# Kernel tuning notes

Hardware: AMD Instinct MI355X
Metric: run time of the kernel (lower is better)

## Reference

```python
import jax, jax.numpy as jnp
import numpy as np

N, E, B = 50000, 800000, 2000
EMB, FEAT, L, NTASK = 300, 512, 5, 1
EPS = 1e-5


def setup_inputs() -> dict:
    key = jax.random.key(0)
    ks = jax.random.split(key, 40)
    s = 0.05
    d = {
        'x': jax.random.randint(ks[0], (N, 42), 0, 3),
        'edge_index': jax.random.randint(ks[1], (2, E), 0, N),
        'edge_attr': jax.random.randint(ks[2], (E, 10), 0, 3),
        'batch': jnp.sort(jax.random.randint(ks[3], (N,), 0, B)),
        'x_add': jax.random.normal(ks[4], (B, 200), jnp.float32),
        # atom embeddings
        'atom_e1': jax.random.normal(ks[5], (120, EMB), jnp.float32) * s,
        'atom_e2': jax.random.normal(ks[6], (3, EMB), jnp.float32) * s,
        'atom_w3': jax.random.normal(ks[7], (40, EMB), jnp.float32) * s,
        'atom_b3': jnp.zeros((EMB,), jnp.float32),
        # per-layer GINEConv params (stacked over L layers)
        'edge_e1': jax.random.normal(ks[8], (L, 6, EMB), jnp.float32) * s,
        'edge_e2': jax.random.normal(ks[9], (L, 4, EMB), jnp.float32) * s,
        'edge_w3': jax.random.normal(ks[10], (L, 8, EMB), jnp.float32) * s,
        'edge_b3': jnp.zeros((L, EMB), jnp.float32),
        'mlp_w1': jax.random.normal(ks[11], (L, EMB, 2 * EMB), jnp.float32) * s,
        'mlp_b1': jnp.zeros((L, 2 * EMB), jnp.float32),
        'mlp_w2': jax.random.normal(ks[12], (L, 2 * EMB, EMB), jnp.float32) * s,
        'mlp_b2': jnp.zeros((L, EMB), jnp.float32),
        'bn_g': jnp.ones((L, EMB), jnp.float32),
        'bn_b': jnp.zeros((L, EMB), jnp.float32),
        # feat_lin: emb_dim + 200 -> feat_dim
        'feat_w': jax.random.normal(ks[13], (EMB + 200, FEAT), jnp.float32) * s,
        'feat_b': jnp.zeros((FEAT,), jnp.float32),
        # pred head: 512->256 softplus, 256->256 softplus, 256->1
        'pw1': jax.random.normal(ks[14], (FEAT, FEAT // 2), jnp.float32) * s,
        'pb1': jnp.zeros((FEAT // 2,), jnp.float32),
        'pw2': jax.random.normal(ks[15], (FEAT // 2, FEAT // 2), jnp.float32) * s,
        'pb2': jnp.zeros((FEAT // 2,), jnp.float32),
        'pw3': jax.random.normal(ks[16], (FEAT // 2, NTASK), jnp.float32) * s,
        'pb3': jnp.zeros((NTASK,), jnp.float32),
    }
    return d


def reference(x, edge_index, edge_attr, batch, x_add,
              atom_e1, atom_e2, atom_w3, atom_b3,
              edge_e1, edge_e2, edge_w3, edge_b3,
              mlp_w1, mlp_b1, mlp_w2, mlp_b2, bn_g, bn_b,
              feat_w, feat_b, pw1, pb1, pw2, pb2, pw3, pb3):
    n = x.shape[0]
    nb = x_add.shape[0]

    # node embedding: emb(atom_type) + emb(chirality) + Linear(40 float feats)
    h = (atom_e1[x[:, 0]] + atom_e2[x[:, 1]]
         + x[:, 2:].astype(jnp.float32) @ atom_w3 + atom_b3)

    # add self loops once (same for every layer); self-loop attr: col0=4, rest 0
    loop = jnp.arange(n, dtype=edge_index.dtype)
    src = jnp.concatenate([edge_index[0], loop])
    dst = jnp.concatenate([edge_index[1], loop])
    ea0 = jnp.concatenate([edge_attr[:, 0], jnp.full((n,), 4, edge_attr.dtype)])
    ea1 = jnp.concatenate([edge_attr[:, 1], jnp.zeros((n,), edge_attr.dtype)])
    eaf = jnp.concatenate([edge_attr[:, 2:].astype(jnp.float32),
                           jnp.zeros((n, 8), jnp.float32)], axis=0)

    for l in range(L):
        e_emb = edge_e1[l][ea0] + edge_e2[l][ea1] + eaf @ edge_w3[l] + edge_b3[l]
        msg = h[src] + e_emb                              # [E+N, EMB] gather
        agg = jax.ops.segment_sum(msg, dst, num_segments=n)  # scatter-add
        h = jnp.maximum(agg @ mlp_w1[l] + mlp_b1[l], 0.0) @ mlp_w2[l] + mlp_b2[l]
        # BatchNorm1d (training-mode batch stats, biased var)
        mu = jnp.mean(h, axis=0)
        var = jnp.mean((h - mu) ** 2, axis=0)
        h = (h - mu) * jax.lax.rsqrt(var + EPS) * bn_g[l] + bn_b[l]
        if l != L - 1:
            h = jnp.maximum(h, 0.0)
    h_node = h

    # global mean pool per graph
    sums = jax.ops.segment_sum(h_node, batch, num_segments=nb)
    cnt = jax.ops.segment_sum(jnp.ones((n, 1), h_node.dtype), batch, num_segments=nb)
    pooled = sums / jnp.maximum(cnt, 1.0)

    g = jnp.concatenate([pooled, x_add], axis=1) @ feat_w + feat_b
    g = jax.nn.softplus(g @ pw1 + pb1)
    g = jax.nn.softplus(g @ pw2 + pb2)
    pred = g @ pw3 + pb3
    return h_node, pred
```

## Files before the change

kernel.cpp:

```cpp
#include <hip/hip_runtime.h>
#include <stdint.h>

#define NN 50000
#define EE 800000
#define BG 2000
#define EMB 300
#define HP 320
#define YP 640
#define MPAD 50048
#define MHEAD 2048
#define NLAYER 5

typedef __attribute__((ext_vector_type(8))) _Float16 f16x8;
typedef __attribute__((ext_vector_type(4))) float f32x4;

__device__ __forceinline__ _Float16 f2h(float f) { return (_Float16)f; }

__global__ void k_tconv_all(const float* __restrict__ mw1, const float* __restrict__ mw2,
        const float* __restrict__ fw, const float* __restrict__ pw1, const float* __restrict__ pw2,
        _Float16* __restrict__ w1t, _Float16* __restrict__ w2t, _Float16* __restrict__ fwt,
        _Float16* __restrict__ p1t, _Float16* __restrict__ p2t) {
    int job = blockIdx.x;
    const float* src; _Float16* dst; int K, Ns, Kp, Np;
    if (job < 5)       { src = mw1 + (size_t)job * EMB * 2 * EMB; dst = w1t + (size_t)job * YP * HP; K = EMB; Ns = 2 * EMB; Kp = HP; Np = YP; }
    else if (job < 10) { int l = job - 5; src = mw2 + (size_t)l * 2 * EMB * EMB; dst = w2t + (size_t)l * HP * YP; K = 2 * EMB; Ns = EMB; Kp = YP; Np = HP; }
    else if (job == 10){ src = fw;  dst = fwt; K = 500; Ns = 512; Kp = 512; Np = 512; }
    else if (job == 11){ src = pw1; dst = p1t; K = 512; Ns = 256; Kp = 512; Np = 256; }
    else               { src = pw2; dst = p2t; K = 256; Ns = 256; Kp = 256; Np = 256; }
    int total = Kp * Np;
    for (int idx = blockIdx.y * 256 + threadIdx.x; idx < total; idx += gridDim.y * 256) {
        int n = idx / Kp, k = idx - n * Kp;
        float v = (n < Ns && k < K) ? src[(size_t)k * Ns + n] : 0.f;
        dst[idx] = f2h(v);
    }
}

__global__ void k_padbias_all(const float* __restrict__ mb1, const float* __restrict__ mb2,
                              float* __restrict__ b1p, float* __restrict__ b2p) {
    int idx = blockIdx.x * 256 + threadIdx.x;
    if (idx < NLAYER * YP) {
        int l = idx / YP, c = idx - l * YP;
        b1p[idx] = (c < 2 * EMB) ? mb1[(size_t)l * 2 * EMB + c] : 0.f;
    } else if (idx < NLAYER * YP + NLAYER * HP) {
        int j = idx - NLAYER * YP; int l = j / HP, c = j - l * HP;
        b2p[j] = (c < EMB) ? mb2[(size_t)l * EMB + c] : 0.f;
    }
}

__global__ void k_prep(int* __restrict__ deg, int* __restrict__ cursor,
                       float* __restrict__ psum, float* __restrict__ psq,
                       float* __restrict__ scl, float* __restrict__ sft) {
    int i = blockIdx.x * blockDim.x + threadIdx.x;
    if (i < NN) { deg[i] = 0; cursor[i] = 0; }
    if (i < HP) { psum[i] = 0.f; psq[i] = 0.f; scl[i] = 1.f; sft[i] = 0.f; }
}

__global__ __launch_bounds__(320) void k_embed(const int* __restrict__ x,
        const float* __restrict__ ae1, const float* __restrict__ ae2,
        const float* __restrict__ aw3, const float* __restrict__ ab3,
        _Float16* __restrict__ h2) {
    int i = blockIdx.x, tid = threadIdx.x;
    __shared__ int sx[42];
    if (tid < 42) sx[tid] = x[(size_t)i * 42 + tid];
    __syncthreads();
    if (tid < EMB) {
        float v = ab3[tid] + ae1[(size_t)sx[0] * EMB + tid] + ae2[(size_t)sx[1] * EMB + tid];
        #pragma unroll 8
        for (int j = 0; j < 40; j++) v += (float)sx[2 + j] * aw3[(size_t)j * EMB + tid];
        h2[(size_t)i * HP + tid] = f2h(v);
    } else {
        h2[(size_t)i * HP + tid] = (_Float16)0.f;
    }
}

__global__ void k_deg(const int* __restrict__ ei, int* __restrict__ deg) {
    int e = blockIdx.x * blockDim.x + threadIdx.x;
    if (e < EE) atomicAdd(&deg[ei[EE + e]], 1);
}

__global__ __launch_bounds__(1024) void k_scan(const int* __restrict__ deg,
                                               int* __restrict__ rowptr) {
    __shared__ int part[1024];
    int t = threadIdx.x;
    const int chunk = (NN + 1023) / 1024;
    int i0 = t * chunk;
    int i1 = min(i0 + chunk, NN);
    int s = 0;
    for (int i = i0; i < i1; i++) s += deg[i];
    part[t] = s;
    __syncthreads();
    for (int off = 1; off < 1024; off <<= 1) {
        int v = part[t];
        int u = (t >= off) ? part[t - off] : 0;
        __syncthreads();
        part[t] = v + u;
        __syncthreads();
    }
    int run = (t > 0) ? part[t - 1] : 0;
    for (int i = i0; i < i1; i++) { rowptr[i] = run; run += deg[i]; }
    if (t == 1023) rowptr[NN] = part[1023];
}

__global__ void k_fill(const int* __restrict__ ei, const int* __restrict__ ea,
                       const int* __restrict__ rowptr, int* __restrict__ cursor,
                       int* __restrict__ col, unsigned int* __restrict__ eattr) {
    int e = blockIdx.x * blockDim.x + threadIdx.x;
    if (e < EE) {
        int d = ei[EE + e];
        int pos = rowptr[d] + atomicAdd(&cursor[d], 1);
        col[pos] = ei[e];
        unsigned int p = (unsigned int)ea[e * 10 + 0] | ((unsigned int)ea[e * 10 + 1] << 2);
        #pragma unroll
        for (int j = 0; j < 8; j++) p |= (unsigned int)ea[e * 10 + 2 + j] << (4 + 2 * j);
        eattr[pos] = p;
    }
}

__global__ __launch_bounds__(256) void k_stats(const int* __restrict__ rowptr,
        const unsigned int* __restrict__ eattr, int* __restrict__ stat) {
    int node = blockIdx.x * 4 + (threadIdx.x >> 6);
    int lane = threadIdx.x & 63;
    if (node >= NN) return;
    int beg = rowptr[node], end = rowptr[node + 1];
    int c0 = 0, c1 = 0, c2 = 0, d1 = 0, d2 = 0;
    int s[8] = {0, 0, 0, 0, 0, 0, 0, 0};
    for (int e = beg + lane; e < end; e += 64) {
        unsigned int p = eattr[e];
        unsigned int a0 = p & 3u, a1 = (p >> 2) & 3u;
        c0 += (a0 == 0); c1 += (a0 == 1); c2 += (a0 == 2);
        d1 += (a1 == 1); d2 += (a1 == 2);
        #pragma unroll
        for (int j = 0; j < 8; j++) s[j] += (int)((p >> (4 + 2 * j)) & 3u);
    }
    #pragma unroll
    for (int off = 32; off; off >>= 1) {
        c0 += __shfl_down(c0, off); c1 += __shfl_down(c1, off); c2 += __shfl_down(c2, off);
        d1 += __shfl_down(d1, off); d2 += __shfl_down(d2, off);
        #pragma unroll
        for (int j = 0; j < 8; j++) s[j] += __shfl_down(s[j], off);
    }
    if (lane == 0) {
        int dg = end - beg;
        int* st = stat + (size_t)node * 20;
        st[0] = c0; st[1] = c1; st[2] = c2; st[3] = 0; st[4] = 1; st[5] = 0;
        st[6] = dg - d1 - d2 + 1; st[7] = d1; st[8] = d2; st[9] = 0;
        #pragma unroll
        for (int j = 0; j < 8; j++) st[10 + j] = s[j];
        st[18] = dg + 1; st[19] = 0;
    }
}

__global__ __launch_bounds__(320) void k_agg(const _Float16* __restrict__ h2,
        const float* __restrict__ scl, const float* __restrict__ sft, int dorelu,
        const int* __restrict__ stat, const int* __restrict__ rowptr,
        const int* __restrict__ col,
        const float* __restrict__ ee1, const float* __restrict__ ee2,
        const float* __restrict__ ew3, const float* __restrict__ eb3,
        _Float16* __restrict__ agg, int layer) {
    int i = blockIdx.x;
    int tid = threadIdx.x;
    if (i >= NN) { agg[(size_t)i * HP + tid] = (_Float16)0.f; return; }
    __shared__ int ss[20];
    if (tid < 20) ss[tid] = stat[(size_t)i * 20 + tid];
    float sc_ = scl[tid], sf_ = sft[tid];
    __syncthreads();
    int c = tid;
    bool act = c < EMB;
    float acc = 0.f;
    if (act) {
        const float* e1 = ee1 + (size_t)layer * 6 * EMB;
        const float* e2 = ee2 + (size_t)layer * 4 * EMB;
        const float* w3 = ew3 + (size_t)layer * 8 * EMB;
        float v = eb3[(size_t)layer * EMB + c] * (float)ss[18];
        #pragma unroll
        for (int k = 0; k < 6; k++) v += (float)ss[k] * e1[k * EMB + c];
        #pragma unroll
        for (int k = 0; k < 4; k++) v += (float)ss[6 + k] * e2[k * EMB + c];
        #pragma unroll
        for (int j = 0; j < 8; j++) v += (float)ss[10 + j] * w3[j * EMB + c];
        float hv = (float)h2[(size_t)i * HP + c];
        float t = fmaf(hv, sc_, sf_);
        if (dorelu) t = fmaxf(t, 0.f);
        acc = v + t;
        int beg = rowptr[i], end = rowptr[i + 1];
        #pragma unroll 4
        for (int e = beg; e < end; ++e) {
            int sid = col[e];
            float v2 = (float)h2[(size_t)sid * HP + c];
            float t2 = fmaf(v2, sc_, sf_);
            if (dorelu) t2 = fmaxf(t2, 0.f);
            acc += t2;
        }
    }
    agg[(size_t)i * HP + tid] = act ? f2h(acc) : (_Float16)0.f;
}

__global__ __launch_bounds__(256) void k_gemm(const _Float16* __restrict__ A, int lda,
        const _Float16* __restrict__ Wt, int ldw, const float* __restrict__ bias,
        _Float16* __restrict__ C, int ldc, int K, int act,
        float* __restrict__ psum, float* __restrict__ psq) {
    __shared__ _Float16 As[128 * 32];
    __shared__ _Float16 Bs[64 * 32];
    int tid = threadIdx.x;
    int lane = tid & 63;
    int wid = tid >> 6;
    int wr = wid >> 1, wc = wid & 1;
    size_t rowBase = (size_t)blockIdx.x * 128;
    int colBase = blockIdx.y * 64;

    int srow = tid >> 2;
    int schunk = tid & 3;
    const _Float16* Ab  = A + (rowBase + srow) * (size_t)lda + (schunk << 3);
    const _Float16* Ab2 = Ab + (size_t)64 * lda;
    const _Float16* Bb  = Wt + ((size_t)colBase + srow) * ldw + (schunk << 3);
    int swz = ((schunk ^ ((srow >> 1) & 3)) << 3);
    int wa0 = srow * 32 + swz;
    int wa1 = wa0 + 64 * 32;
    int wb  = wa0;

    uint4 ra0 = *(const uint4*)Ab;
    uint4 ra1 = *(const uint4*)Ab2;
    uint4 rb  = *(const uint4*)Bb;

    int lr = lane & 15, lg = lane >> 4;
    int lswz = (lr >> 1) & 3;
    int aoff[4], boff[2];
    #pragma unroll
    for (int m = 0; m < 4; m++) { int r = wr * 64 + m * 16 + lr; aoff[m] = r * 32 + ((lg ^ lswz) << 3); }
    #pragma unroll
    for (int n = 0; n < 2; n++) { int r = wc * 32 + n * 16 + lr; boff[n] = r * 32 + ((lg ^ lswz) << 3); }

    f32x4 acc[4][2];
    #pragma unroll
    for (int m = 0; m < 4; m++)
        #pragma unroll
        for (int n = 0; n < 2; n++) acc[m][n] = (f32x4){0.f, 0.f, 0.f, 0.f};

    int nk = K >> 5;
    for (int kt = 0; kt < nk; ++kt) {
        __syncthreads();
        *(uint4*)&As[wa0] = ra0;
        *(uint4*)&As[wa1] = ra1;
        *(uint4*)&Bs[wb]  = rb;
        __syncthreads();
        if (kt + 1 < nk) {
            int o = (kt + 1) << 5;
            ra0 = *(const uint4*)(Ab + o);
            ra1 = *(const uint4*)(Ab2 + o);
            rb  = *(const uint4*)(Bb + o);
        }
        f16x8 af[4], bfr[2];
        #pragma unroll
        for (int m = 0; m < 4; m++) af[m] = *(const f16x8*)&As[aoff[m]];
        #pragma unroll
        for (int n = 0; n < 2; n++) bfr[n] = *(const f16x8*)&Bs[boff[n]];
        #pragma unroll
        for (int m = 0; m < 4; m++)
            #pragma unroll
            for (int n = 0; n < 2; n++)
                acc[m][n] = __builtin_amdgcn_mfma_f32_16x16x32_f16(af[m], bfr[n], acc[m][n], 0, 0, 0);
    }

    bool dostats = (psum != nullptr);
    float sstat[2] = {0.f, 0.f}, qstat[2] = {0.f, 0.f};
    #pragma unroll
    for (int m = 0; m < 4; m++) {
        #pragma unroll
        for (int n = 0; n < 2; n++) {
            int colg = colBase + wc * 32 + n * 16 + lr;
            float bv = bias[colg];
            #pragma unroll
            for (int r = 0; r < 4; r++) {
                size_t rowg = rowBase + wr * 64 + m * 16 + lg * 4 + r;
                float v = acc[m][n][r] + bv;
                if (act == 1) v = fmaxf(v, 0.f);
                else if (act == 2) v = (v > 0.f) ? v + log1pf(expf(-v)) : log1pf(expf(v));
                C[rowg * ldc + colg] = f2h(v);
                if (dostats && rowg < NN) { sstat[n] += v; qstat[n] += v * v; }
            }
        }
    }
    if (dostats) {
        #pragma unroll
        for (int n = 0; n < 2; n++) {
            float s_ = sstat[n], q_ = qstat[n];
            s_ += __shfl_xor(s_, 16); q_ += __shfl_xor(q_, 16);
            s_ += __shfl_xor(s_, 32); q_ += __shfl_xor(q_, 32);
            if (lane < 16) {
                int colg = colBase + wc * 32 + n * 16 + lr;
                atomicAdd(&psum[colg], s_);
                atomicAdd(&psq[colg], q_);
            }
        }
    }
}

__global__ __launch_bounds__(320) void k_bn_final(float* __restrict__ psum,
        float* __restrict__ psq, const float* __restrict__ bng,
        const float* __restrict__ bnb, float* __restrict__ scl, float* __restrict__ sft,
        int layer) {
    int c = threadIdx.x;
    float s = psum[c], q = psq[c];
    float* so = scl + (size_t)(layer + 1) * HP;
    float* fo = sft + (size_t)(layer + 1) * HP;
    if (c < EMB) {
        float mu = s / (float)NN;
        float var = q / (float)NN - mu * mu;
        float rstd = rsqrtf(var + 1e-5f);
        float g = bng[(size_t)layer * EMB + c] * rstd;
        so[c] = g;
        fo[c] = bnb[(size_t)layer * EMB + c] - mu * g;
    } else { so[c] = 0.f; fo[c] = 0.f; }
    psum[c] = 0.f; psq[c] = 0.f;
}

__global__ __launch_bounds__(320) void k_bn_apply(const _Float16* __restrict__ h2,
        const float* __restrict__ scl, const float* __restrict__ sft,
        float* __restrict__ out) {
    int i = blockIdx.x, c = threadIdx.x;
    if (c < EMB)
        out[(size_t)i * EMB + c] = fmaf((float)h2[(size_t)i * HP + c], scl[c], sft[c]);
}

__global__ __launch_bounds__(320) void k_pool(const float* __restrict__ hn,
        const int* __restrict__ batch, float* __restrict__ pooled) {
    __shared__ int sb[2];
    if (threadIdx.x < 2) {
        int target = blockIdx.x + threadIdx.x;
        int lo = 0, hi = NN;
        while (lo < hi) { int mid = (lo + hi) >> 1; if (batch[mid] < target) lo = mid + 1; else hi = mid; }
        sb[threadIdx.x] = lo;
    }
    __syncthreads();
    int s = sb[0], e = sb[1], c = threadIdx.x;
    if (c < EMB) {
        float acc = 0.f;
        for (int i = s; i < e; i++) acc += hn[(size_t)i * EMB + c];
        float inv = 1.f / (float)max(e - s, 1);
        pooled[(size_t)blockIdx.x * EMB + c] = acc * inv;
    }
}

__global__ __launch_bounds__(512) void k_head_in(const float* __restrict__ pooled,
        const float* __restrict__ x_add, _Float16* __restrict__ hin) {
    int b = blockIdx.x, c = threadIdx.x;
    float v = 0.f;
    if (b < BG) {
        if (c < EMB) v = pooled[(size_t)b * EMB + c];
        else if (c < EMB + 200) v = x_add[(size_t)b * 200 + (c - EMB)];
    }
    hin[(size_t)b * 512 + c] = f2h(v);
}

__global__ __launch_bounds__(64) void k_pred(const _Float16* __restrict__ g3,
        const float* __restrict__ pw3, const float* __restrict__ pb3, float* __restrict__ out) {
    int row = blockIdx.x;
    int lane = threadIdx.x;
    float s = 0.f;
    #pragma unroll
    for (int t = 0; t < 4; t++) {
        int k = lane * 4 + t;
        s += (float)g3[(size_t)row * 256 + k] * pw3[k];
    }
    #pragma unroll
    for (int off = 32; off; off >>= 1) s += __shfl_down(s, off);
    if (lane == 0) out[row] = s + pb3[0];
}

extern "C" void kernel_launch(void* const* d_in, const int* in_sizes, int n_in,
                              void* d_out, int out_size, void* d_ws, size_t ws_size,
                              hipStream_t stream) {
    const int*   x     = (const int*)d_in[0];
    const int*   ei    = (const int*)d_in[1];
    const int*   ea    = (const int*)d_in[2];
    const int*   batch = (const int*)d_in[3];
    const float* x_add = (const float*)d_in[4];
    const float* ae1   = (const float*)d_in[5];
    const float* ae2   = (const float*)d_in[6];
    const float* aw3   = (const float*)d_in[7];
    const float* ab3   = (const float*)d_in[8];
    const float* ee1   = (const float*)d_in[9];
    const float* ee2   = (const float*)d_in[10];
    const float* ew3   = (const float*)d_in[11];
    const float* eb3   = (const float*)d_in[12];
    const float* mw1   = (const float*)d_in[13];
    const float* mb1   = (const float*)d_in[14];
    const float* mw2   = (const float*)d_in[15];
    const float* mb2   = (const float*)d_in[16];
    const float* bng   = (const float*)d_in[17];
    const float* bnb   = (const float*)d_in[18];
    const float* fw    = (const float*)d_in[19];
    const float* fb    = (const float*)d_in[20];
    const float* pw1   = (const float*)d_in[21];
    const float* pb1   = (const float*)d_in[22];
    const float* pw2   = (const float*)d_in[23];
    const float* pb2   = (const float*)d_in[24];
    const float* pw3   = (const float*)d_in[25];
    const float* pb3   = (const float*)d_in[26];
    (void)in_sizes; (void)n_in; (void)out_size; (void)ws_size;
    float* out = (float*)d_out;

    char* p = (char*)d_ws;
    auto take = [&](size_t bytes) -> char* {
        char* r = p; p += (bytes + 255) & ~(size_t)255; return r;
    };
    _Float16*  h2   = (_Float16*)take((size_t)MPAD * HP * 2);
    _Float16*  agg  = (_Float16*)take((size_t)MPAD * HP * 2);
    _Float16*  y1   = (_Float16*)take((size_t)MPAD * YP * 2);
    _Float16*  w1t  = (_Float16*)take((size_t)NLAYER * YP * HP * 2);
    _Float16*  w2t  = (_Float16*)take((size_t)NLAYER * HP * YP * 2);
    _Float16*  fwt  = (_Float16*)take((size_t)512 * 512 * 2);
    _Float16*  p1t  = (_Float16*)take((size_t)256 * 512 * 2);
    _Float16*  p2t  = (_Float16*)take((size_t)256 * 256 * 2);
    float* b1p    = (float*)take((size_t)NLAYER * YP * 4);
    float* b2p    = (float*)take((size_t)NLAYER * HP * 4);
    int* deg      = (int*)take((size_t)NN * 4);
    int* cursor   = (int*)take((size_t)NN * 4);
    int* rowptr   = (int*)take((size_t)(NN + 1) * 4);
    int* col      = (int*)take((size_t)EE * 4);
    unsigned int* eattr = (unsigned int*)take((size_t)EE * 4);
    int* stat     = (int*)take((size_t)NN * 20 * 4);
    float* psum   = (float*)take((size_t)HP * 4);
    float* psq    = (float*)take((size_t)HP * 4);
    float* scl    = (float*)take((size_t)(NLAYER + 1) * HP * 4);
    float* sft    = (float*)take((size_t)(NLAYER + 1) * HP * 4);
    float* pooled = (float*)take((size_t)BG * EMB * 4);
    char* hb = (char*)y1;
    _Float16* hin = (_Float16*)hb;  hb += (size_t)MHEAD * 512 * 2;
    _Float16* g1  = (_Float16*)hb;  hb += (size_t)MHEAD * 512 * 2;
    _Float16* g2  = (_Float16*)hb;  hb += (size_t)MHEAD * 256 * 2;
    _Float16* g3  = (_Float16*)hb;

    k_prep<<<(NN + 255) / 256, 256, 0, stream>>>(deg, cursor, psum, psq, scl, sft);
    k_tconv_all<<<dim3(13, 1024), 256, 0, stream>>>(mw1, mw2, fw, pw1, pw2, w1t, w2t, fwt, p1t, p2t);
    k_padbias_all<<<19, 256, 0, stream>>>(mb1, mb2, b1p, b2p);
    k_embed<<<NN, 320, 0, stream>>>(x, ae1, ae2, aw3, ab3, h2);
    k_deg<<<(EE + 255) / 256, 256, 0, stream>>>(ei, deg);
    k_scan<<<1, 1024, 0, stream>>>(deg, rowptr);
    k_fill<<<(EE + 255) / 256, 256, 0, stream>>>(ei, ea, rowptr, cursor, col, eattr);
    k_stats<<<(NN + 3) / 4, 256, 0, stream>>>(rowptr, eattr, stat);

    for (int l = 0; l < NLAYER; l++) {
        k_agg<<<MPAD, 320, 0, stream>>>(h2, scl + (size_t)l * HP, sft + (size_t)l * HP,
            (l > 0) ? 1 : 0, stat, rowptr, col, ee1, ee2, ew3, eb3, agg, l);
        k_gemm<<<dim3(MPAD / 128, YP / 64), 256, 0, stream>>>(
            agg, HP, w1t + (size_t)l * YP * HP, HP, b1p + (size_t)l * YP, y1, YP, HP, 1,
            nullptr, nullptr);
        k_gemm<<<dim3(MPAD / 128, HP / 64), 256, 0, stream>>>(
            y1, YP, w2t + (size_t)l * HP * YP, YP, b2p + (size_t)l * HP, h2, HP, YP, 0,
            psum, psq);
        k_bn_final<<<1, 320, 0, stream>>>(psum, psq, bng, bnb, scl, sft, l);
    }
    k_bn_apply<<<NN, 320, 0, stream>>>(h2, scl + (size_t)NLAYER * HP, sft + (size_t)NLAYER * HP, out);

    k_pool<<<BG, 320, 0, stream>>>(out, batch, pooled);
    k_head_in<<<MHEAD, 512, 0, stream>>>(pooled, x_add, hin);
    k_gemm<<<dim3(MHEAD / 128, 512 / 64), 256, 0, stream>>>(hin, 512, fwt, 512, fb, g1, 512, 512, 0, nullptr, nullptr);
    k_gemm<<<dim3(MHEAD / 128, 256 / 64), 256, 0, stream>>>(g1, 512, p1t, 512, pb1, g2, 256, 512, 2, nullptr, nullptr);
    k_gemm<<<dim3(MHEAD / 128, 256 / 64), 256, 0, stream>>>(g2, 256, p2t, 256, pb2, g3, 256, 256, 2, nullptr, nullptr);
    k_pred<<<BG, 64, 0, stream>>>(g3, pw3, pb3, out + (size_t)NN * EMB);
}
```

Measured before the change: 2.035 ms.

## Double-buffer GEMM with direct global-to-LDS loads, wave-per-node aggregation, fold BN finalize

The GEMM now double-buffers its LDS tiles, fills them with global_load_lds so the next K-tile loads while MFMAs run, and remaps workgroups so contiguous tiles land on the same XCD. The aggregation and embedding kernels switch from one 320-thread block per node to one 64-lane wave per node, and the neighbour loop is unrolled by four for more loads in flight. The BatchNorm finalize kernel is removed: each consumer recomputes scale and shift from per-layer partial-sum buffers. Pooling and head-input assembly are fused into one kernel. The main risks are redundant per-wave BN recomputation and the correctness of the swizzled direct-to-LDS addressing.

```diff
diff --git a/kernel.cpp b/kernel.cpp
--- a/kernel.cpp
+++ b/kernel.cpp
@@ -48,28 +48,46 @@
 }
 
 __global__ void k_prep(int* __restrict__ deg, int* __restrict__ cursor,
-                       float* __restrict__ psum, float* __restrict__ psq,
-                       float* __restrict__ scl, float* __restrict__ sft) {
+                       float* __restrict__ psum, float* __restrict__ psq) {
     int i = blockIdx.x * blockDim.x + threadIdx.x;
     if (i < NN) { deg[i] = 0; cursor[i] = 0; }
-    if (i < HP) { psum[i] = 0.f; psq[i] = 0.f; scl[i] = 1.f; sft[i] = 0.f; }
-}
-
-__global__ __launch_bounds__(320) void k_embed(const int* __restrict__ x,
+    if (i < NLAYER * HP) { psum[i] = 0.f; psq[i] = 0.f; }
+}
+
+__global__ __launch_bounds__(256) void k_embed(const int* __restrict__ x,
         const float* __restrict__ ae1, const float* __restrict__ ae2,
         const float* __restrict__ aw3, const float* __restrict__ ab3,
         _Float16* __restrict__ h2) {
-    int i = blockIdx.x, tid = threadIdx.x;
-    __shared__ int sx[42];
-    if (tid < 42) sx[tid] = x[(size_t)i * 42 + tid];
-    __syncthreads();
-    if (tid < EMB) {
-        float v = ab3[tid] + ae1[(size_t)sx[0] * EMB + tid] + ae2[(size_t)sx[1] * EMB + tid];
-        #pragma unroll 8
-        for (int j = 0; j < 40; j++) v += (float)sx[2 + j] * aw3[(size_t)j * EMB + tid];
-        h2[(size_t)i * HP + tid] = f2h(v);
-    } else {
-        h2[(size_t)i * HP + tid] = (_Float16)0.f;
+    int node = blockIdx.x * 4 + (threadIdx.x >> 6);
+    int lane = threadIdx.x & 63;
+    if (node >= MPAD) return;
+    _Float16* outr = h2 + (size_t)node * HP;
+    if (node >= NN) {
+        #pragma unroll
+        for (int j = 0; j < 5; j++) outr[lane + 64 * j] = (_Float16)0.f;
+        return;
+    }
+    const int* xr = x + (size_t)node * 42;
+    int x0 = xr[0], x1 = xr[1];
+    float acc[5];
+    #pragma unroll
+    for (int j = 0; j < 5; j++) {
+        int c = lane + 64 * j;
+        acc[j] = (j < 4 || c < EMB)
+               ? (ab3[c] + ae1[(size_t)x0 * EMB + c] + ae2[(size_t)x1 * EMB + c]) : 0.f;
+    }
+    for (int k = 0; k < 40; k++) {
+        float xv = (float)xr[2 + k];
+        #pragma unroll
+        for (int j = 0; j < 5; j++) {
+            int c = lane + 64 * j;
+            if (j < 4 || c < EMB) acc[j] = fmaf(xv, aw3[(size_t)k * EMB + c], acc[j]);
+        }
+    }
+    #pragma unroll
+    for (int j = 0; j < 5; j++) {
+        int c = lane + 64 * j;
+        outr[c] = (j < 4 || c < EMB) ? f2h(acc[j]) : (_Float16)0.f;
     }
 }
 
@@ -150,85 +168,156 @@
     }
 }
 
-__global__ __launch_bounds__(320) void k_agg(const _Float16* __restrict__ h2,
-        const float* __restrict__ scl, const float* __restrict__ sft, int dorelu,
+__global__ __launch_bounds__(256) void k_agg(const _Float16* __restrict__ h2,
+        const float* __restrict__ psum, const float* __restrict__ psq,
+        const float* __restrict__ bng, const float* __restrict__ bnb,
         const int* __restrict__ stat, const int* __restrict__ rowptr,
         const int* __restrict__ col,
         const float* __restrict__ ee1, const float* __restrict__ ee2,
         const float* __restrict__ ew3, const float* __restrict__ eb3,
         _Float16* __restrict__ agg, int layer) {
-    int i = blockIdx.x;
-    int tid = threadIdx.x;
-    if (i >= NN) { agg[(size_t)i * HP + tid] = (_Float16)0.f; return; }
-    __shared__ int ss[20];
-    if (tid < 20) ss[tid] = stat[(size_t)i * 20 + tid];
-    float sc_ = scl[tid], sf_ = sft[tid];
-    __syncthreads();
-    int c = tid;
-    bool act = c < EMB;
-    float acc = 0.f;
-    if (act) {
-        const float* e1 = ee1 + (size_t)layer * 6 * EMB;
-        const float* e2 = ee2 + (size_t)layer * 4 * EMB;
-        const float* w3 = ew3 + (size_t)layer * 8 * EMB;
-        float v = eb3[(size_t)layer * EMB + c] * (float)ss[18];
-        #pragma unroll
-        for (int k = 0; k < 6; k++) v += (float)ss[k] * e1[k * EMB + c];
-        #pragma unroll
-        for (int k = 0; k < 4; k++) v += (float)ss[6 + k] * e2[k * EMB + c];
-        #pragma unroll
-        for (int j = 0; j < 8; j++) v += (float)ss[10 + j] * w3[j * EMB + c];
-        float hv = (float)h2[(size_t)i * HP + c];
-        float t = fmaf(hv, sc_, sf_);
-        if (dorelu) t = fmaxf(t, 0.f);
-        acc = v + t;
-        int beg = rowptr[i], end = rowptr[i + 1];
-        #pragma unroll 4
-        for (int e = beg; e < end; ++e) {
-            int sid = col[e];
-            float v2 = (float)h2[(size_t)sid * HP + c];
-            float t2 = fmaf(v2, sc_, sf_);
-            if (dorelu) t2 = fmaxf(t2, 0.f);
-            acc += t2;
-        }
-    }
-    agg[(size_t)i * HP + tid] = act ? f2h(acc) : (_Float16)0.f;
+    int node = blockIdx.x * 4 + (threadIdx.x >> 6);
+    int lane = threadIdx.x & 63;
+    if (node >= MPAD) return;
+    _Float16* outr = agg + (size_t)node * HP;
+    if (node >= NN) {
+        #pragma unroll
+        for (int j = 0; j < 5; j++) outr[lane + 64 * j] = (_Float16)0.f;
+        return;
+    }
+    float sc[5], sf[5];
+    #pragma unroll
+    for (int j = 0; j < 5; j++) { sc[j] = 1.f; sf[j] = 0.f; }
+    int dorelu = (layer > 0);
+    if (layer > 0) {
+        const float* ps = psum + (size_t)(layer - 1) * HP;
+        const float* pq = psq  + (size_t)(layer - 1) * HP;
+        const float* g_ = bng + (size_t)(layer - 1) * EMB;
+        const float* b_ = bnb + (size_t)(layer - 1) * EMB;
+        #pragma unroll
+        for (int j = 0; j < 5; j++) {
+            int c = lane + 64 * j;
+            if (j < 4 || c < EMB) {
+                float mu = ps[c] * (1.f / NN);
+                float var = pq[c] * (1.f / NN) - mu * mu;
+                float g = g_[c] * rsqrtf(var + 1e-5f);
+                sc[j] = g; sf[j] = b_[c] - mu * g;
+            }
+        }
+    }
+    const int* st = stat + (size_t)node * 20;
+    const float* e1 = ee1 + (size_t)layer * 6 * EMB;
+    const float* e2 = ee2 + (size_t)layer * 4 * EMB;
+    const float* w3 = ew3 + (size_t)layer * 8 * EMB;
+    const float* b3 = eb3 + (size_t)layer * EMB;
+    float s18 = (float)st[18];
+    float st0 = (float)st[0], st1 = (float)st[1], st2 = (float)st[2];
+    float st6 = (float)st[6], st7 = (float)st[7], st8 = (float)st[8];
+    float sw[8];
+    #pragma unroll
+    for (int k = 0; k < 8; k++) sw[k] = (float)st[10 + k];
+    float acc[5];
+    #pragma unroll
+    for (int j = 0; j < 5; j++) {
+        int c = lane + 64 * j;
+        float v = 0.f;
+        if (j < 4 || c < EMB) {
+            v = b3[c] * s18 + e1[4 * EMB + c];
+            v = fmaf(st0, e1[c], v);
+            v = fmaf(st1, e1[EMB + c], v);
+            v = fmaf(st2, e1[2 * EMB + c], v);
+            v = fmaf(st6, e2[c], v);
+            v = fmaf(st7, e2[EMB + c], v);
+            v = fmaf(st8, e2[2 * EMB + c], v);
+            #pragma unroll
+            for (int k = 0; k < 8; k++) v = fmaf(sw[k], w3[k * EMB + c], v);
+        }
+        acc[j] = v;
+    }
+    {
+        const _Float16* pr = h2 + (size_t)node * HP;
+        #pragma unroll
+        for (int j = 0; j < 5; j++) {
+            int c = lane + 64 * j;
+            if (j < 4 || c < EMB) {
+                float t = fmaf((float)pr[c], sc[j], sf[j]);
+                if (dorelu) t = fmaxf(t, 0.f);
+                acc[j] += t;
+            }
+        }
+    }
+    int beg = rowptr[node], end = rowptr[node + 1];
+    int e = beg;
+    for (; e + 4 <= end; e += 4) {
+        const _Float16* p0 = h2 + (size_t)col[e]     * HP;
+        const _Float16* p1 = h2 + (size_t)col[e + 1] * HP;
+        const _Float16* p2 = h2 + (size_t)col[e + 2] * HP;
+        const _Float16* p3 = h2 + (size_t)col[e + 3] * HP;
+        #pragma unroll
+        for (int j = 0; j < 5; j++) {
+            int c = lane + 64 * j;
+            if (j < 4 || c < EMB) {
+                float t0 = fmaf((float)p0[c], sc[j], sf[j]);
+                float t1 = fmaf((float)p1[c], sc[j], sf[j]);
+                float t2 = fmaf((float)p2[c], sc[j], sf[j]);
+                float t3 = fmaf((float)p3[c], sc[j], sf[j]);
+                if (dorelu) {
+                    t0 = fmaxf(t0, 0.f); t1 = fmaxf(t1, 0.f);
+                    t2 = fmaxf(t2, 0.f); t3 = fmaxf(t3, 0.f);
+                }
+                acc[j] += (t0 + t1) + (t2 + t3);
+            }
+        }
+    }
+    for (; e < end; ++e) {
+        const _Float16* p0 = h2 + (size_t)col[e] * HP;
+        #pragma unroll
+        for (int j = 0; j < 5; j++) {
+            int c = lane + 64 * j;
+            if (j < 4 || c < EMB) {
+                float t = fmaf((float)p0[c], sc[j], sf[j]);
+                if (dorelu) t = fmaxf(t, 0.f);
+                acc[j] += t;
+            }
+        }
+    }
+    #pragma unroll
+    for (int j = 0; j < 5; j++) {
+        int c = lane + 64 * j;
+        outr[c] = (j < 4 || c < EMB) ? f2h(acc[j]) : (_Float16)0.f;
+    }
 }
 
 __global__ __launch_bounds__(256) void k_gemm(const _Float16* __restrict__ A, int lda,
         const _Float16* __restrict__ Wt, int ldw, const float* __restrict__ bias,
-        _Float16* __restrict__ C, int ldc, int K, int act,
+        _Float16* __restrict__ C, int ldc, int K, int act, int gridY,
         float* __restrict__ psum, float* __restrict__ psq) {
-    __shared__ _Float16 As[128 * 32];
-    __shared__ _Float16 Bs[64 * 32];
-    int tid = threadIdx.x;
-    int lane = tid & 63;
-    int wid = tid >> 6;
+    __shared__ _Float16 As[2][128 * 32];
+    __shared__ _Float16 Bs[2][64 * 32];
+    int nwg = gridDim.x;
+    int q = nwg >> 3, r = nwg & 7;
+    int xcd = blockIdx.x & 7, idx = blockIdx.x >> 3;
+    int wg = ((xcd < r) ? xcd * (q + 1) : r * (q + 1) + (xcd - r) * q) + idx;
+    int bx = wg / gridY, by = wg - bx * gridY;
+    size_t rowBase = (size_t)bx * 128;
+    int colBase = by * 64;
+
+    int tid = threadIdx.x, lane = tid & 63, wid = tid >> 6;
     int wr = wid >> 1, wc = wid & 1;
-    size_t rowBase = (size_t)blockIdx.x * 128;
-    int colBase = blockIdx.y * 64;
-
-    int srow = tid >> 2;
-    int schunk = tid & 3;
-    const _Float16* Ab  = A + (rowBase + srow) * (size_t)lda + (schunk << 3);
+    int srow = tid >> 2, schunk = tid & 3;
+    int gchunk = schunk ^ ((srow >> 1) & 3);
+    const _Float16* Ab  = A + (rowBase + srow) * (size_t)lda + (gchunk << 3);
     const _Float16* Ab2 = Ab + (size_t)64 * lda;
-    const _Float16* Bb  = Wt + ((size_t)colBase + srow) * ldw + (schunk << 3);
-    int swz = ((schunk ^ ((srow >> 1) & 3)) << 3);
-    int wa0 = srow * 32 + swz;
-    int wa1 = wa0 + 64 * 32;
-    int wb  = wa0;
-
-    uint4 ra0 = *(const uint4*)Ab;
-    uint4 ra1 = *(const uint4*)Ab2;
-    uint4 rb  = *(const uint4*)Bb;
+    const _Float16* Bb  = Wt + ((size_t)colBase + srow) * ldw + (gchunk << 3);
+    int ldsbase = wid << 9;
 
     int lr = lane & 15, lg = lane >> 4;
     int lswz = (lr >> 1) & 3;
     int aoff[4], boff[2];
     #pragma unroll
-    for (int m = 0; m < 4; m++) { int r = wr * 64 + m * 16 + lr; aoff[m] = r * 32 + ((lg ^ lswz) << 3); }
-    #pragma unroll
-    for (int n = 0; n < 2; n++) { int r = wc * 32 + n * 16 + lr; boff[n] = r * 32 + ((lg ^ lswz) << 3); }
+    for (int m = 0; m < 4; m++) { int rr = wr * 64 + m * 16 + lr; aoff[m] = rr * 32 + ((lg ^ lswz) << 3); }
+    #pragma unroll
+    for (int n = 0; n < 2; n++) { int rr = wc * 32 + n * 16 + lr; boff[n] = rr * 32 + ((lg ^ lswz) << 3); }
 
     f32x4 acc[4][2];
     #pragma unroll
@@ -236,29 +325,37 @@
         #pragma unroll
         for (int n = 0; n < 2; n++) acc[m][n] = (f32x4){0.f, 0.f, 0.f, 0.f};
 
+    auto stage = [&](int buf, int kt) {
+        int o = kt << 5;
+        __builtin_amdgcn_global_load_lds(
+            (const __attribute__((address_space(1))) void*)(Ab + o),
+            (__attribute__((address_space(3))) void*)&As[buf][ldsbase], 16, 0, 0);
+        __builtin_amdgcn_global_load_lds(
+            (const __attribute__((address_space(1))) void*)(Ab2 + o),
+            (__attribute__((address_space(3))) void*)&As[buf][64 * 32 + ldsbase], 16, 0, 0);
+        __builtin_amdgcn_global_load_lds(
+            (const __attribute__((address_space(1))) void*)(Bb + o),
+            (__attribute__((address_space(3))) void*)&Bs[buf][ldsbase], 16, 0, 0);
+    };
+
     int nk = K >> 5;
+    stage(0, 0);
+    __syncthreads();
+    int cur = 0;
     for (int kt = 0; kt < nk; ++kt) {
-        __syncthreads();
-        *(uint4*)&As[wa0] = ra0;
-        *(uint4*)&As[wa1] = ra1;
-        *(uint4*)&Bs[wb]  = rb;
-        __syncthreads();
-        if (kt + 1 < nk) {
-            int o = (kt + 1) << 5;
-            ra0 = *(const uint4*)(Ab + o);
-            ra1 = *(const uint4*)(Ab2 + o);
-            rb  = *(const uint4*)(Bb + o);
-        }
+        if (kt + 1 < nk) stage(cur ^ 1, kt + 1);
         f16x8 af[4], bfr[2];
         #pragma unroll
-        for (int m = 0; m < 4; m++) af[m] = *(const f16x8*)&As[aoff[m]];
-        #pragma unroll
-        for (int n = 0; n < 2; n++) bfr[n] = *(const f16x8*)&Bs[boff[n]];
+        for (int m = 0; m < 4; m++) af[m] = *(const f16x8*)&As[cur][aoff[m]];
+        #pragma unroll
+        for (int n = 0; n < 2; n++) bfr[n] = *(const f16x8*)&Bs[cur][boff[n]];
         #pragma unroll
         for (int m = 0; m < 4; m++)
             #pragma unroll
             for (int n = 0; n < 2; n++)
                 acc[m][n] = __builtin_amdgcn_mfma_f32_16x16x32_f16(af[m], bfr[n], acc[m][n], 0, 0, 0);
+        __syncthreads();
+        cur ^= 1;
     }
 
     bool dostats = (psum != nullptr);
@@ -270,9 +367,9 @@
             int colg = colBase + wc * 32 + n * 16 + lr;
             float bv = bias[colg];
             #pragma unroll
-            for (int r = 0; r < 4; r++) {
-                size_t rowg = rowBase + wr * 64 + m * 16 + lg * 4 + r;
-                float v = acc[m][n][r] + bv;
+            for (int rj = 0; rj < 4; rj++) {
+                size_t rowg = rowBase + wr * 64 + m * 16 + lg * 4 + rj;
+                float v = acc[m][n][rj] + bv;
                 if (act == 1) v = fmaxf(v, 0.f);
                 else if (act == 2) v = (v > 0.f) ? v + log1pf(expf(-v)) : log1pf(expf(v));
                 C[rowg * ldc + colg] = f2h(v);
@@ -295,59 +392,51 @@
     }
 }
 
-__global__ __launch_bounds__(320) void k_bn_final(float* __restrict__ psum,
-        float* __restrict__ psq, const float* __restrict__ bng,
-        const float* __restrict__ bnb, float* __restrict__ scl, float* __restrict__ sft,
-        int layer) {
-    int c = threadIdx.x;
-    float s = psum[c], q = psq[c];
-    float* so = scl + (size_t)(layer + 1) * HP;
-    float* fo = sft + (size_t)(layer + 1) * HP;
-    if (c < EMB) {
-        float mu = s / (float)NN;
-        float var = q / (float)NN - mu * mu;
-        float rstd = rsqrtf(var + 1e-5f);
-        float g = bng[(size_t)layer * EMB + c] * rstd;
-        so[c] = g;
-        fo[c] = bnb[(size_t)layer * EMB + c] - mu * g;
-    } else { so[c] = 0.f; fo[c] = 0.f; }
-    psum[c] = 0.f; psq[c] = 0.f;
-}
-
-__global__ __launch_bounds__(320) void k_bn_apply(const _Float16* __restrict__ h2,
-        const float* __restrict__ scl, const float* __restrict__ sft,
+__global__ __launch_bounds__(256) void k_bn_apply(const _Float16* __restrict__ h2,
+        const float* __restrict__ psum, const float* __restrict__ psq,
+        const float* __restrict__ bng, const float* __restrict__ bnb,
         float* __restrict__ out) {
-    int i = blockIdx.x, c = threadIdx.x;
-    if (c < EMB)
-        out[(size_t)i * EMB + c] = fmaf((float)h2[(size_t)i * HP + c], scl[c], sft[c]);
-}
-
-__global__ __launch_bounds__(320) void k_pool(const float* __restrict__ hn,
-        const int* __restrict__ batch, float* __restrict__ pooled) {
+    int node = blockIdx.x * 4 + (threadIdx.x >> 6);
+    int lane = threadIdx.x & 63;
+    if (node >= NN) return;
+    const float* ps = psum + (size_t)(NLAYER - 1) * HP;
+    const float* pq = psq  + (size_t)(NLAYER - 1) * HP;
+    const float* g_ = bng + (size_t)(NLAYER - 1) * EMB;
+    const float* b_ = bnb + (size_t)(NLAYER - 1) * EMB;
+    #pragma unroll
+    for (int j = 0; j < 5; j++) {
+        int c = lane + 64 * j;
+        if (j < 4 || c < EMB) {
+            float mu = ps[c] * (1.f / NN);
+            float var = pq[c] * (1.f / NN) - mu * mu;
+            float g = g_[c] * rsqrtf(var + 1e-5f);
+            out[(size_t)node * EMB + c] =
+                fmaf((float)h2[(size_t)node * HP + c], g, b_[c] - mu * g);
+        }
+    }
+}
+
+__global__ __launch_bounds__(512) void k_pool(const float* __restrict__ hn,
+        const int* __restrict__ batch, const float* __restrict__ x_add,
+        _Float16* __restrict__ hin) {
+    int b = blockIdx.x, c = threadIdx.x;
+    if (b >= BG) { hin[(size_t)b * 512 + c] = (_Float16)0.f; return; }
     __shared__ int sb[2];
-    if (threadIdx.x < 2) {
-        int target = blockIdx.x + threadIdx.x;
+    if (c < 2) {
+        int target = b + c;
         int lo = 0, hi = NN;
         while (lo < hi) { int mid = (lo + hi) >> 1; if (batch[mid] < target) lo = mid + 1; else hi = mid; }
-        sb[threadIdx.x] = lo;
+        sb[c] = lo;
     }
     __syncthreads();
-    int s = sb[0], e = sb[1], c = threadIdx.x;
+    float v = 0.f;
     if (c < EMB) {
-        float acc = 0.f;
-        for (int i = s; i < e; i++) acc += hn[(size_t)i * EMB + c];
-        float inv = 1.f / (float)max(e - s, 1);
-        pooled[(size_t)blockIdx.x * EMB + c] = acc * inv;
-    }
-}
-
-__global__ __launch_bounds__(512) void k_head_in(const float* __restrict__ pooled,
-        const float* __restrict__ x_add, _Float16* __restrict__ hin) {
-    int b = blockIdx.x, c = threadIdx.x;
-    float v = 0.f;
-    if (b < BG) {
-        if (c < EMB) v = pooled[(size_t)b * EMB + c];
-        else if (c < EMB + 200) v = x_add[(size_t)b * 200 + (c - EMB)];
+        int s = sb[0], e = sb[1];
+        float a = 0.f;
+        for (int i = s; i < e; i++) a += hn[(size_t)i * EMB + c];
+        v = a / (float)max(e - s, 1);
+    } else if (c < EMB + 200) {
+        v = x_add[(size_t)b * 200 + (c - EMB)];
     }
     hin[(size_t)b * 512 + c] = f2h(v);
 }
@@ -420,43 +509,39 @@
     int* col      = (int*)take((size_t)EE * 4);
     unsigned int* eattr = (unsigned int*)take((size_t)EE * 4);
     int* stat     = (int*)take((size_t)NN * 20 * 4);
-    float* psum   = (float*)take((size_t)HP * 4);
-    float* psq    = (float*)take((size_t)HP * 4);
-    float* scl    = (float*)take((size_t)(NLAYER + 1) * HP * 4);
-    float* sft    = (float*)take((size_t)(NLAYER + 1) * HP * 4);
-    float* pooled = (float*)take((size_t)BG * EMB * 4);
+    float* psum   = (float*)take((size_t)NLAYER * HP * 4);
+    float* psq    = (float*)take((size_t)NLAYER * HP * 4);
     char* hb = (char*)y1;
     _Float16* hin = (_Float16*)hb;  hb += (size_t)MHEAD * 512 * 2;
     _Float16* g1  = (_Float16*)hb;  hb += (size_t)MHEAD * 512 * 2;
     _Float16* g2  = (_Float16*)hb;  hb += (size_t)MHEAD * 256 * 2;
     _Float16* g3  = (_Float16*)hb;
 
-    k_prep<<<(NN + 255) / 256, 256, 0, stream>>>(deg, cursor, psum, psq, scl, sft);
+    k_prep<<<(NN + 255) / 256, 256, 0, stream>>>(deg, cursor, psum, psq);
     k_tconv_all<<<dim3(13, 1024), 256, 0, stream>>>(mw1, mw2, fw, pw1, pw2, w1t, w2t, fwt, p1t, p2t);
     k_padbias_all<<<19, 256, 0, stream>>>(mb1, mb2, b1p, b2p);
-    k_embed<<<NN, 320, 0, stream>>>(x, ae1, ae2, aw3, ab3, h2);
+    k_embed<<<(MPAD + 3) / 4, 256, 0, stream>>>(x, ae1, ae2, aw3, ab3, h2);
     k_deg<<<(EE + 255) / 256, 256, 0, stream>>>(ei, deg);
     k_scan<<<1, 1024, 0, stream>>>(deg, rowptr);
     k_fill<<<(EE + 255) / 256, 256, 0, stream>>>(ei, ea, rowptr, cursor, col, eattr);
     k_stats<<<(NN + 3) / 4, 256, 0, stream>>>(rowptr, eattr, stat);
 
+    const int MT = MPAD / 128;
     for (int l = 0; l < NLAYER; l++) {
-        k_agg<<<MPAD, 320, 0, stream>>>(h2, scl + (size_t)l * HP, sft + (size_t)l * HP,
-            (l > 0) ? 1 : 0, stat, rowptr, col, ee1, ee2, ew3, eb3, agg, l);
-        k_gemm<<<dim3(MPAD / 128, YP / 64), 256, 0, stream>>>(
-            agg, HP, w1t + (size_t)l * YP * HP, HP, b1p + (size_t)l * YP, y1, YP, HP, 1,
-            nullptr, nullptr);
-        k_gemm<<<dim3(MPAD / 128, HP / 64), 256, 0, stream>>>(
-            y1, YP, w2t + (size_t)l * HP * YP, YP, b2p + (size_t)l * HP, h2, HP, YP, 0,
-            psum, psq);
-        k_bn_final<<<1, 320, 0, stream>>>(psum, psq, bng, bnb, scl, sft, l);
-    }
-    k_bn_apply<<<NN, 320, 0, stream>>>(h2, scl + (size_t)NLAYER * HP, sft + (size_t)NLAYER * HP, out);
-
-    k_pool<<<BG, 320, 0, stream>>>(out, batch, pooled);
-    k_head_in<<<MHEAD, 512, 0, stream>>>(pooled, x_add, hin);
-    k_gemm<<<dim3(MHEAD / 128, 512 / 64), 256, 0, stream>>>(hin, 512, fwt, 512, fb, g1, 512, 512, 0, nullptr, nullptr);
-    k_gemm<<<dim3(MHEAD / 128, 256 / 64), 256, 0, stream>>>(g1, 512, p1t, 512, pb1, g2, 256, 512, 2, nullptr, nullptr);
-    k_gemm<<<dim3(MHEAD / 128, 256 / 64), 256, 0, stream>>>(g2, 256, p2t, 256, pb2, g3, 256, 256, 2, nullptr, nullptr);
+        k_agg<<<(MPAD + 3) / 4, 256, 0, stream>>>(h2, psum, psq, bng, bnb,
+            stat, rowptr, col, ee1, ee2, ew3, eb3, agg, l);
+        k_gemm<<<MT * (YP / 64), 256, 0, stream>>>(
+            agg, HP, w1t + (size_t)l * YP * HP, HP, b1p + (size_t)l * YP,
+            y1, YP, HP, 1, YP / 64, nullptr, nullptr);
+        k_gemm<<<MT * (HP / 64), 256, 0, stream>>>(
+            y1, YP, w2t + (size_t)l * HP * YP, YP, b2p + (size_t)l * HP,
+            h2, HP, YP, 0, HP / 64, psum + (size_t)l * HP, psq + (size_t)l * HP);
+    }
+    k_bn_apply<<<(NN + 3) / 4, 256, 0, stream>>>(h2, psum, psq, bng, bnb, out);
+
+    k_pool<<<MHEAD, 512, 0, stream>>>(out, batch, x_add, hin);
+    k_gemm<<<(MHEAD / 128) * (512 / 64), 256, 0, stream>>>(hin, 512, fwt, 512, fb, g1, 512, 512, 0, 512 / 64, nullptr, nullptr);
+    k_gemm<<<(MHEAD / 128) * (256 / 64), 256, 0, stream>>>(g1, 512, p1t, 512, pb1, g2, 256, 512, 2, 256 / 64, nullptr, nullptr);
+    k_gemm<<<(MHEAD / 128) * (256 / 64), 256, 0, stream>>>(g2, 256, p2t, 256, pb2, g3, 256, 256, 2, 256 / 64, nullptr, nullptr);
     k_pred<<<BG, 64, 0, stream>>>(g3, pw3, pb3, out + (size_t)NN * EMB);
 }
```

New measurement: 2.169 ms. +6.6%, slower.
